# Optimization experiments

Measured on AMD Instinct MI355X. Metric: run time of the kernel, lower is better.

The kernel has to match this reference:

```python
import jax, jax.numpy as jnp
import numpy as np

B, T, D, H = 8192, 128, 16, 32
EPS = 1e-5  # BatchNorm1d default eps (eval mode, running stats)


def setup_inputs() -> dict:
    key = jax.random.key(0)
    ks = iter(jax.random.split(key, 64))

    def nrm(shape, s=0.1):
        return jax.random.normal(next(ks), shape, jnp.float32) * s

    inp = {}
    inp["S"] = nrm((B, T, D), 1.0)
    inp["g_S"] = nrm((B, T), 1.0)
    inp["times"] = jnp.linspace(0.0, 1.0, T, dtype=jnp.float32)
    inp["payoff_T"] = nrm((B,), 1.0)
    inp["delta_T"] = nrm((B, D), 1.0)
    # init_hidden: uniform(-0.1, 0.1), shape [num_layers=2, B, H]
    inp["h_price0"] = jax.random.uniform(next(ks), (2, B, H), jnp.float32, -0.1, 0.1)
    inp["h_delta0"] = jax.random.uniform(next(ks), (2, B, H), jnp.float32, -0.1, 0.1)
    # params for price net (prefix p_, out_dim=1) and delta net (prefix d_, out_dim=D)
    for pfx, out_dim in (("p", 1), ("d", D)):
        inp[pfx + "_Wih0"] = nrm((3 * H, 2 * D))
        inp[pfx + "_Whh0"] = nrm((3 * H, H))
        inp[pfx + "_bih0"] = nrm((3 * H,))
        inp[pfx + "_bhh0"] = nrm((3 * H,))
        inp[pfx + "_Wih1"] = nrm((3 * H, H))
        inp[pfx + "_Whh1"] = nrm((3 * H, H))
        inp[pfx + "_bih1"] = nrm((3 * H,))
        inp[pfx + "_bhh1"] = nrm((3 * H,))
        inp[pfx + "_embW"] = nrm((H, H))
        inp[pfx + "_embB"] = nrm((H,))
        inp[pfx + "_bng"] = jnp.ones((H,), jnp.float32)
        inp[pfx + "_bnb"] = jnp.zeros((H,), jnp.float32)
        inp[pfx + "_bnm"] = nrm((H,))
        inp[pfx + "_bnv"] = jax.random.uniform(next(ks), (H,), jnp.float32, 0.5, 1.5)
        inp[pfx + "_outW"] = nrm((out_dim, H))
        inp[pfx + "_outB"] = nrm((out_dim,))
    return inp


def _gru_cell(x, h, Wih, Whh, bih, bhh):
    # PyTorch GRU cell, gate order (r, z, n)
    gi = x @ Wih.T + bih
    gh = h @ Whh.T + bhh
    ir, iz, inn = jnp.split(gi, 3, axis=-1)
    hr, hz, hn = jnp.split(gh, 3, axis=-1)
    r = jax.nn.sigmoid(ir + hr)
    z = jax.nn.sigmoid(iz + hz)
    n = jnp.tanh(inn + r * hn)
    return (1.0 - z) * n + z * h


def _head(y, Wemb, bemb, g, b, m, v, Wout, bout, sig):
    # Linear -> BatchNorm1d (eval, running stats) -> SiLU -> Linear [-> Sigmoid]
    e = y @ Wemb.T + bemb
    e = (e - m) * jax.lax.rsqrt(v + EPS) * g + b
    e = e * jax.nn.sigmoid(e)  # SiLU
    o = e @ Wout.T + bout
    return jax.nn.sigmoid(o) if sig else o


def reference(S, g_S, times, payoff_T, delta_T, h_price0, h_delta0,
              p_Wih0, p_Whh0, p_bih0, p_bhh0, p_Wih1, p_Whh1, p_bih1, p_bhh1,
              p_embW, p_embB, p_bng, p_bnb, p_bnm, p_bnv, p_outW, p_outB,
              d_Wih0, d_Whh0, d_bih0, d_bhh0, d_Wih1, d_Whh1, d_bih1, d_bhh1,
              d_embW, d_embB, d_bng, d_bnb, d_bnm, d_bnv, d_outW, d_outB):
    # X = cat([S, g_S expanded to d]) -> [B, T, 2D]
    gS = jnp.broadcast_to(g_S[..., None], S.shape)
    X = jnp.concatenate([S, gS], axis=-1)
    Xr = jnp.swapaxes(X, 0, 1)[::-1]  # [T, B, 2D], time reversed (loop goes t=T-1..0)

    def step(carry, xt):
        hp0, hp1, hd0, hd1 = carry
        hp0 = _gru_cell(xt, hp0, p_Wih0, p_Whh0, p_bih0, p_bhh0)
        hp1 = _gru_cell(hp0, hp1, p_Wih1, p_Whh1, p_bih1, p_bhh1)
        hd0 = _gru_cell(xt, hd0, d_Wih0, d_Whh0, d_bih0, d_bhh0)
        hd1 = _gru_cell(hd0, hd1, d_Wih1, d_Whh1, d_bih1, d_bhh1)
        return (hp0, hp1, hd0, hd1), (hp1, hd1)

    carry0 = (h_price0[0], h_price0[1], h_delta0[0], h_delta0[1])
    _, (Yp, Yd) = jax.lax.scan(step, carry0, Xr)
    # flip time back to forward order: outputs were collected for t=T-1..0
    Yp = jnp.swapaxes(Yp[::-1], 0, 1)  # [B, T, H]
    Yd = jnp.swapaxes(Yd[::-1], 0, 1)  # [B, T, H]
    prices = _head(Yp, p_embW, p_embB, p_bng, p_bnb, p_bnm, p_bnv, p_outW, p_outB, False)  # [B,T,1]
    deltas = _head(Yd, d_embW, d_embB, d_bng, d_bnb, d_bnm, d_bnv, d_outW, d_outB, True)   # [B,T,D]
    return (prices, deltas)
```

## Files before the change

### kernel.cpp

```cpp
#include <hip/hip_runtime.h>
#include <hip/hip_bf16.h>
#include <stdint.h>

#define DI __device__ __forceinline__

typedef float f32x4 __attribute__((ext_vector_type(4)));
typedef float f32x2 __attribute__((ext_vector_type(2)));
typedef short bf16x8 __attribute__((ext_vector_type(8)));

constexpr int BB = 8192, TT = 128, DD = 16, HH = 32;
constexpr float kEPS = 1e-5f;
constexpr float kLOG2E = 1.44269504088896340736f;

DI float rcpf_(float x) { return __builtin_amdgcn_rcpf(x); }
DI float exp2f_(float x) { return __builtin_amdgcn_exp2f(x); }
DI float sigm(float x) { return rcpf_(1.0f + exp2f_(-kLOG2E * x)); }

DI uint32_t cvtpk(float lo, float hi) {
  uint32_t r;
  asm("v_cvt_pk_bf16_f32 %0, %1, %2" : "=v"(r) : "v"(lo), "v"(hi));
  return r;
}

DI f32x4 mfma_(bf16x8 a, bf16x8 b, f32x4 c) {
  return __builtin_amdgcn_mfma_f32_16x16x32_bf16(a, b, c, 0, 0, 0);
}

union U4 { uint4 q; bf16x8 v; uint32_t u[4]; };

__global__ void prep_net(const float* Wih0, const float* Whh0,
                         const float* bih0, const float* bhh0,
                         const float* Wih1, const float* Whh1,
                         const float* bih1, const float* bhh1,
                         const float* embW, const float* embB,
                         const float* bng, const float* bnb,
                         const float* bnm, const float* bnv,
                         const float* outW, const float* outB,
                         int outDim, uint8_t* wsbase) {
  int tid = threadIdx.x;
  uint16_t* W = (uint16_t*)wsbase;
  float* bias = (float*)(wsbase + 27648);
  auto cvt = [](float f) -> uint16_t {
    union { float f; uint32_t u; } v; v.f = f;
    uint32_t u = v.u;
    return (uint16_t)((u + 0x7FFF + ((u >> 16) & 1)) >> 16);
  };
  const float oscale = (outDim == 16) ? -kLOG2E : 1.0f;
  for (int idx = tid; idx < 27 * 64; idx += 256) {
    int tile = idx >> 6, l = idx & 63, cc = l & 15, gg = l >> 4;
    uint16_t* dst = W + (size_t)idx * 8;
    if (tile < 24) {
      const float* mats[4] = {Wih0, Whh0, Wih1, Whh1};
      const float* src = mats[tile / 6];
      int sub = tile % 6;
      int row = sub * 16 + cc;
      float sc = (sub < 4) ? -kLOG2E : 2.0f * kLOG2E;
#pragma unroll
      for (int j = 0; j < 8; ++j) {
        int k = (j < 4) ? 4 * gg + j : 16 + 4 * gg + (j - 4);
        dst[j] = cvt(src[row * 32 + k] * sc);
      }
    } else if (tile < 26) {
      int row = (tile - 24) * 16 + cc;
      float a = bng[row] * rsqrtf(bnv[row] + kEPS);
#pragma unroll
      for (int j = 0; j < 8; ++j) {
        int k = (j < 4) ? 4 * gg + j : 16 + 4 * gg + (j - 4);
        dst[j] = cvt(embW[row * 32 + k] * a);
      }
    } else {
      int rrow = (cc < outDim) ? cc : 0;
      float sc = (cc < outDim) ? oscale : 0.0f;
#pragma unroll
      for (int j = 0; j < 8; ++j) {
        int k = (j < 4) ? 4 * gg + j : 16 + 4 * gg + (j - 4);
        dst[j] = cvt(outW[rrow * 32 + k] * sc);
      }
    }
  }
  for (int idx = tid; idx < 304; idx += 256) {
    int tile = idx >> 4, n = idx & 15;
    float v;
    if (tile < 8) {
      if (tile < 4)      v = (bih0[tile * 16 + n] + bhh0[tile * 16 + n]) * (-kLOG2E);
      else if (tile < 6) v = bih0[64 + (tile - 4) * 16 + n] * (2.0f * kLOG2E);
      else               v = bhh0[64 + (tile - 6) * 16 + n] * (2.0f * kLOG2E);
    } else if (tile < 16) {
      int tt = tile - 8;
      if (tt < 4)        v = (bih1[tt * 16 + n] + bhh1[tt * 16 + n]) * (-kLOG2E);
      else if (tt < 6)   v = bih1[64 + (tt - 4) * 16 + n] * (2.0f * kLOG2E);
      else               v = bhh1[64 + (tt - 6) * 16 + n] * (2.0f * kLOG2E);
    } else if (tile < 18) {
      int nn = (tile - 16) * 16 + n;
      float a = bng[nn] * rsqrtf(bnv[nn] + kEPS);
      v = a * (embB[nn] - bnm[nn]) + bnb[nn];
    } else {
      v = (n < outDim) ? outB[n] * oscale : 0.0f;
    }
    bias[idx] = v;
  }
}

__global__ __launch_bounds__(64, 1) void rnn_fused(
    const float* __restrict__ S, const float* __restrict__ gS,
    const float* __restrict__ hp0, const float* __restrict__ hd0,
    const uint8_t* __restrict__ ws, float* __restrict__ out) {
  const int lane = threadIdx.x & 63;
  const int net = blockIdx.x & 1;
  const int b0 = (blockIdx.x >> 1) * 16;
  const int c = lane & 15, g = lane >> 4;

  const uint16_t* W = (const uint16_t*)(ws + net * 32768);
  const float* bias = (const float*)(ws + net * 32768 + 27648);
  const float* hsrc = net ? hd0 : hp0;

  bf16x8 Wt[27];
#pragma unroll
  for (int t = 0; t < 27; ++t)
    Wt[t] = *(const bf16x8*)(W + (t * 64 + lane) * 8);
  f32x4 Bq[19];
#pragma unroll
  for (int t = 0; t < 19; ++t)
    Bq[t] = *(const f32x4*)(bias + t * 16 + 4 * g);

  auto packB = [&](const float (&v)[8]) -> bf16x8 {
    U4 t;
    t.u[0] = cvtpk(v[0], v[1]); t.u[1] = cvtpk(v[2], v[3]);
    t.u[2] = cvtpk(v[4], v[5]); t.u[3] = cvtpk(v[6], v[7]);
    return t.v;
  };

  auto mfmaGRU = [&](int wih, int whh, int bb, bf16x8 xf, bf16x8 hf,
                     f32x4 (&A)[8]) {
    A[0] = mfma_(Wt[wih + 0], xf, Bq[bb + 0]); A[0] = mfma_(Wt[whh + 0], hf, A[0]);
    A[1] = mfma_(Wt[wih + 1], xf, Bq[bb + 1]); A[1] = mfma_(Wt[whh + 1], hf, A[1]);
    A[2] = mfma_(Wt[wih + 2], xf, Bq[bb + 2]); A[2] = mfma_(Wt[whh + 2], hf, A[2]);
    A[3] = mfma_(Wt[wih + 3], xf, Bq[bb + 3]); A[3] = mfma_(Wt[whh + 3], hf, A[3]);
    A[4] = mfma_(Wt[wih + 4], xf, Bq[bb + 4]);
    A[5] = mfma_(Wt[wih + 5], xf, Bq[bb + 5]);
    A[6] = mfma_(Wt[whh + 4], hf, Bq[bb + 6]);
    A[7] = mfma_(Wt[whh + 5], hf, Bq[bb + 7]);
  };

  auto gates = [&](const f32x4 (&A)[8], float (&hC)[8]) {
    const f32x2 one = {1.0f, 1.0f};
#pragma unroll
    for (int r = 0; r < 4; ++r) {
      f32x2 ra = {A[0][r], A[1][r]};
      f32x2 za = {A[2][r], A[3][r]};
      f32x2 ni = {A[4][r], A[5][r]};
      f32x2 nh = {A[6][r], A[7][r]};
      f32x2 hv = {hC[r], hC[4 + r]};
      f32x2 era = {exp2f_(ra[0]), exp2f_(ra[1])};
      f32x2 t1 = one + era;
      f32x2 rg = {rcpf_(t1[0]), rcpf_(t1[1])};
      f32x2 w = ni + rg * nh;
      f32x2 En = {exp2f_(w[0]), exp2f_(w[1])};
      f32x2 Ez = {exp2f_(za[0]), exp2f_(za[1])};
      f32x2 num = (hv - Ez) + En * (hv + Ez);
      f32x2 den = (one + En) * (one + Ez);
      f32x2 rd = {rcpf_(den[0]), rcpf_(den[1])};
      f32x2 res = num * rd;
      hC[r] = res[0]; hC[4 + r] = res[1];
    }
  };

  auto silu = [&](const f32x4& e0, const f32x4& e1, float (&es)[8]) {
#pragma unroll
    for (int r = 0; r < 4; ++r) {
      float a = e0[r], b = e1[r];
      es[r]     = a * sigm(a);
      es[4 + r] = b * sigm(b);
    }
  };

  auto storeO = [&](const f32x4& o, int th) {
    if (net == 0) {
      if (lane < 16) out[(size_t)(b0 + c) * TT + th] = o[0];
    } else {
      f32x4 so;
#pragma unroll
      for (int r = 0; r < 4; ++r) so[r] = rcpf_(1.0f + exp2f_(o[r]));
      *(f32x4*)(out + (size_t)BB * TT +
                ((size_t)(b0 + c) * TT + th) * DD + 4 * g) = so;
    }
  };

  auto loadState = [&](const float* row, float (&hC)[8]) -> bf16x8 {
    f32x4 a = *(const f32x4*)(row + 4 * g);
    f32x4 b = *(const f32x4*)(row + 16 + 4 * g);
#pragma unroll
    for (int r = 0; r < 4; ++r) { hC[r] = a[r]; hC[4 + r] = b[r]; }
    U4 t;
    t.u[0] = cvtpk(a[0], a[1]); t.u[1] = cvtpk(a[2], a[3]);
    t.u[2] = cvtpk(b[0], b[1]); t.u[3] = cvtpk(b[2], b[3]);
    return t.v;
  };

  auto mkX = [&](f32x4 sv, float gsv) -> bf16x8 {
    uint32_t pkg = cvtpk(gsv, gsv);
    U4 t;
    t.u[0] = cvtpk(sv[0], sv[1]);
    t.u[1] = cvtpk(sv[2], sv[3]);
    t.u[2] = pkg;
    t.u[3] = pkg;
    return t.v;
  };

  const float* Sbase  = S  + (size_t)(b0 + c) * TT * DD + 4 * g;
  const float* gSbase = gS + (size_t)(b0 + c) * TT;

  float h0C[8], h1C[8], es[8];
  bf16x8 h0B = loadState(hsrc + (size_t)(b0 + c) * HH, h0C);
  bf16x8 h1B = loadState(hsrc + ((size_t)BB + b0 + c) * HH, h1C);
  bf16x8 ef, xB;
  f32x4 A0[8], A1[8], e0, e1, o;

  f32x4 xr0, xr1;
  float gr0, gr1;
  xB  = mkX(*(const f32x4*)(Sbase + (size_t)(TT - 1) * DD), gSbase[TT - 1]);
  xr0 = *(const f32x4*)(Sbase + (size_t)(TT - 2) * DD); gr0 = gSbase[TT - 2];
  xr1 = *(const f32x4*)(Sbase + (size_t)(TT - 3) * DD); gr1 = gSbase[TT - 3];
  auto rollX = [&](int tn) {
    xB = mkX(xr0, gr0);
    xr0 = xr1; gr0 = gr1;
    if (tn < 0) tn = 0;
    xr1 = *(const f32x4*)(Sbase + (size_t)tn * DD); gr1 = gSbase[tn];
  };

  mfmaGRU(0, 6, 0, xB, h0B, A0);
  gates(A0, h0C);
  h0B = packB(h0C);
  rollX(TT - 4);
  mfmaGRU(12, 18, 8, h0B, h1B, A1);
  mfmaGRU(0, 6, 0, xB, h0B, A0);
  gates(A1, h1C);
  gates(A0, h0C);
  h1B = packB(h1C); h0B = packB(h0C);
  rollX(TT - 5);
  mfmaGRU(12, 18, 8, h0B, h1B, A1);
  e0 = mfma_(Wt[24], h1B, Bq[16]);
  e1 = mfma_(Wt[25], h1B, Bq[17]);
  mfmaGRU(0, 6, 0, xB, h0B, A0);
  gates(A1, h1C);
  gates(A0, h0C);
  silu(e0, e1, es);
  h1B = packB(h1C); h0B = packB(h0C); ef = packB(es);
  rollX(TT - 6);

#pragma unroll 1
  for (int t = TT - 4; t >= 0; --t) {
    mfmaGRU(12, 18, 8, h0B, h1B, A1);
    e0 = mfma_(Wt[24], h1B, Bq[16]);
    e1 = mfma_(Wt[25], h1B, Bq[17]);
    o  = mfma_(Wt[26], ef, Bq[18]);
    mfmaGRU(0, 6, 0, xB, h0B, A0);
    __builtin_amdgcn_sched_barrier(0);
    gates(A1, h1C);
    gates(A0, h0C);
    silu(e0, e1, es);
    storeO(o, t + 3);
    __builtin_amdgcn_sched_barrier(0);
    h1B = packB(h1C);
    h0B = packB(h0C);
    ef  = packB(es);
    rollX(t - 3);
  }

  mfmaGRU(12, 18, 8, h0B, h1B, A1);
  e0 = mfma_(Wt[24], h1B, Bq[16]);
  e1 = mfma_(Wt[25], h1B, Bq[17]);
  o  = mfma_(Wt[26], ef, Bq[18]);
  gates(A1, h1C);
  silu(e0, e1, es);
  storeO(o, 2);
  h1B = packB(h1C); ef = packB(es);
  e0 = mfma_(Wt[24], h1B, Bq[16]);
  e1 = mfma_(Wt[25], h1B, Bq[17]);
  o  = mfma_(Wt[26], ef, Bq[18]);
  silu(e0, e1, es);
  storeO(o, 1);
  ef = packB(es);
  o = mfma_(Wt[26], ef, Bq[18]);
  storeO(o, 0);
}

extern "C" void kernel_launch(void* const* d_in, const int* in_sizes, int n_in,
                              void* d_out, int out_size, void* d_ws,
                              size_t ws_size, hipStream_t stream) {
  const float* S   = (const float*)d_in[0];
  const float* gS  = (const float*)d_in[1];
  const float* hp0 = (const float*)d_in[5];
  const float* hd0 = (const float*)d_in[6];
  uint8_t* ws = (uint8_t*)d_ws;

  prep_net<<<1, 256, 0, stream>>>(
      (const float*)d_in[7],  (const float*)d_in[8],  (const float*)d_in[9],
      (const float*)d_in[10], (const float*)d_in[11], (const float*)d_in[12],
      (const float*)d_in[13], (const float*)d_in[14], (const float*)d_in[15],
      (const float*)d_in[16], (const float*)d_in[17], (const float*)d_in[18],
      (const float*)d_in[19], (const float*)d_in[20], (const float*)d_in[21],
      (const float*)d_in[22], 1, ws);
  prep_net<<<1, 256, 0, stream>>>(
      (const float*)d_in[23], (const float*)d_in[24], (const float*)d_in[25],
      (const float*)d_in[26], (const float*)d_in[27], (const float*)d_in[28],
      (const float*)d_in[29], (const float*)d_in[30], (const float*)d_in[31],
      (const float*)d_in[32], (const float*)d_in[33], (const float*)d_in[34],
      (const float*)d_in[35], (const float*)d_in[36], (const float*)d_in[37],
      (const float*)d_in[38], 16, ws + 32768);

  rnn_fused<<<dim3((BB / 16) * 2), dim3(64), 0, stream>>>(S, gS, hp0, hd0,
                                                          ws, (float*)d_out);
}
```

Measured before the change: 147.5 us.

## Merge weight-prep kernels and interleave MFMA with VALU via sched group barriers

Combines the two weight-preparation launches into one two-block kernel to save a launch. In the recurrent loop it removes the hard sched_barriers, unrolls by two, and adds sched_group_barrier hints that interleave each MFMA with eight VALU ops. The aim is to hide MFMA latency behind gate, SiLU and pack arithmetic on the serial recurrence path. Looser scheduling and unrolling may raise register pressure or produce a worse ordering than the previous explicit phases.

```diff
diff --git a/kernel.cpp b/kernel.cpp
--- a/kernel.cpp
+++ b/kernel.cpp
@@ -28,15 +28,15 @@
 
 union U4 { uint4 q; bf16x8 v; uint32_t u[4]; };
 
-__global__ void prep_net(const float* Wih0, const float* Whh0,
-                         const float* bih0, const float* bhh0,
-                         const float* Wih1, const float* Whh1,
-                         const float* bih1, const float* bhh1,
-                         const float* embW, const float* embB,
-                         const float* bng, const float* bnb,
-                         const float* bnm, const float* bnv,
-                         const float* outW, const float* outB,
-                         int outDim, uint8_t* wsbase) {
+__device__ void prep_impl(const float* Wih0, const float* Whh0,
+                          const float* bih0, const float* bhh0,
+                          const float* Wih1, const float* Whh1,
+                          const float* bih1, const float* bhh1,
+                          const float* embW, const float* embB,
+                          const float* bng, const float* bnb,
+                          const float* bnm, const float* bnv,
+                          const float* outW, const float* outB,
+                          int outDim, uint8_t* wsbase) {
   int tid = threadIdx.x;
   uint16_t* W = (uint16_t*)wsbase;
   float* bias = (float*)(wsbase + 27648);
@@ -101,6 +101,24 @@
   }
 }
 
+__global__ void prep_both(
+    const float* pW0, const float* pWh0, const float* pb0, const float* pbh0,
+    const float* pW1, const float* pWh1, const float* pb1, const float* pbh1,
+    const float* pe,  const float* peb,  const float* pg,  const float* pbb,
+    const float* pm,  const float* pv,   const float* po,  const float* pob,
+    const float* dW0, const float* dWh0, const float* db0, const float* dbh0,
+    const float* dW1, const float* dWh1, const float* db1, const float* dbh1,
+    const float* de,  const float* deb,  const float* dg,  const float* dbb,
+    const float* dm,  const float* dv,   const float* doW, const float* dob,
+    uint8_t* ws) {
+  if (blockIdx.x == 0)
+    prep_impl(pW0, pWh0, pb0, pbh0, pW1, pWh1, pb1, pbh1,
+              pe, peb, pg, pbb, pm, pv, po, pob, 1, ws);
+  else
+    prep_impl(dW0, dWh0, db0, dbh0, dW1, dWh1, db1, dbh1,
+              de, deb, dg, dbb, dm, dv, doW, dob, 16, ws + 32768);
+}
+
 __global__ __launch_bounds__(64, 1) void rnn_fused(
     const float* __restrict__ S, const float* __restrict__ gS,
     const float* __restrict__ hp0, const float* __restrict__ hd0,
@@ -248,23 +266,26 @@
   h1B = packB(h1C); h0B = packB(h0C); ef = packB(es);
   rollX(TT - 6);
 
-#pragma unroll 1
+#pragma unroll 2
   for (int t = TT - 4; t >= 0; --t) {
     mfmaGRU(12, 18, 8, h0B, h1B, A1);
     e0 = mfma_(Wt[24], h1B, Bq[16]);
     e1 = mfma_(Wt[25], h1B, Bq[17]);
     o  = mfma_(Wt[26], ef, Bq[18]);
     mfmaGRU(0, 6, 0, xB, h0B, A0);
-    __builtin_amdgcn_sched_barrier(0);
     gates(A1, h1C);
     gates(A0, h0C);
     silu(e0, e1, es);
     storeO(o, t + 3);
-    __builtin_amdgcn_sched_barrier(0);
     h1B = packB(h1C);
     h0B = packB(h0C);
     ef  = packB(es);
     rollX(t - 3);
+#pragma unroll
+    for (int kq = 0; kq < 27; ++kq) {
+      __builtin_amdgcn_sched_group_barrier(0x008, 1, 0);
+      __builtin_amdgcn_sched_group_barrier(0x002, 8, 0);
+    }
   }
 
   mfmaGRU(12, 18, 8, h0B, h1B, A1);
@@ -294,20 +315,19 @@
   const float* hd0 = (const float*)d_in[6];
   uint8_t* ws = (uint8_t*)d_ws;
 
-  prep_net<<<1, 256, 0, stream>>>(
+  prep_both<<<2, 256, 0, stream>>>(
       (const float*)d_in[7],  (const float*)d_in[8],  (const float*)d_in[9],
       (const float*)d_in[10], (const float*)d_in[11], (const float*)d_in[12],
       (const float*)d_in[13], (const float*)d_in[14], (const float*)d_in[15],
       (const float*)d_in[16], (const float*)d_in[17], (const float*)d_in[18],
       (const float*)d_in[19], (const float*)d_in[20], (const float*)d_in[21],
-      (const float*)d_in[22], 1, ws);
-  prep_net<<<1, 256, 0, stream>>>(
+      (const float*)d_in[22],
       (const float*)d_in[23], (const float*)d_in[24], (const float*)d_in[25],
       (const float*)d_in[26], (const float*)d_in[27], (const float*)d_in[28],
       (const float*)d_in[29], (const float*)d_in[30], (const float*)d_in[31],
       (const float*)d_in[32], (const float*)d_in[33], (const float*)d_in[34],
       (const float*)d_in[35], (const float*)d_in[36], (const float*)d_in[37],
-      (const float*)d_in[38], 16, ws + 32768);
+      (const float*)d_in[38], ws);
 
   rnn_fused<<<dim3((BB / 16) * 2), dim3(64), 0, stream>>>(S, gS, hp0, hd0,
                                                           ws, (float*)d_out);
```

Result: faster. 140.2 us (median of 2 runs) (-5.0%).
